# Optimization experiments

Hardware: AMD Instinct MI355X
Metric: run time of the kernel (lower is better)

## Reference

```python
import jax, jax.numpy as jnp
import numpy as np

RADIUS = 3
T_STEPS = 2
NEG = -9.0e8
B, L, DEG = 256, 64, 6
FEAT, BOND, FP, OUT = 39, 10, 256, 1


def _leaky(x):
    return jax.nn.leaky_relu(x, 0.01)


def _gru(x, h, wih, whh, bih, bhh):
    # PyTorch GRUCell: gates ordered (r, z, n)
    gi = x @ wih.T + bih
    gh = h @ whh.T + bhh
    ir, iz, inn = jnp.split(gi, 3, axis=-1)
    hr, hz, hn = jnp.split(gh, 3, axis=-1)
    r = jax.nn.sigmoid(ir + hr)
    z = jax.nn.sigmoid(iz + hz)
    n = jnp.tanh(inn + r * hn)
    return (1.0 - z) * n + z * h


def _forward(atom_list, bond_list, atom_mask,
             atom_fc_w, atom_fc_b, neighbor_fc_w, neighbor_fc_b,
             align_w, align_b, attend_w, attend_b,
             gru_wih, gru_whh, gru_bih, gru_bhh,
             mol_align_w, mol_align_b, mol_attend_w, mol_attend_b,
             mol_gru_wih, mol_gru_whh, mol_gru_bih, mol_gru_bhh,
             out_w, out_b,
             atom_degree_list, bond_degree_list):
    b, l, _ = atom_list.shape
    mask = atom_mask[..., None]                                   # [B,L,1]
    atom_feature = _leaky(atom_list @ atom_fc_w.T + atom_fc_b)    # [B,L,FP]

    # per-molecule neighbor gather (padding index = L-1)
    bidx = jnp.arange(b)[:, None, None]
    atom_nb = atom_list[bidx, atom_degree_list]                    # [B,L,deg,FEAT]
    bond_nb = bond_list[bidx, bond_degree_list]                    # [B,L,deg,BOND]
    neighbor_feature = _leaky(
        jnp.concatenate([atom_nb, bond_nb], axis=-1) @ neighbor_fc_w.T + neighbor_fc_b
    )                                                              # [B,L,deg,FP]

    attend_mask = (atom_degree_list != l - 1).astype(atom_feature.dtype)[..., None]
    softmax_mask = jnp.where(atom_degree_list == l - 1, NEG, 0.0).astype(atom_feature.dtype)[..., None]

    for d in range(RADIUS):
        af_exp = jnp.broadcast_to(atom_feature[:, :, None, :], neighbor_feature.shape)
        feature_align = jnp.concatenate([af_exp, neighbor_feature], axis=-1)  # [B,L,deg,2FP]
        align_score = _leaky(feature_align @ align_w[d].T + align_b[d]) + softmax_mask
        attention_weight = jax.nn.softmax(align_score, axis=-2) * attend_mask
        attended = neighbor_feature @ attend_w[d].T + attend_b[d]
        context = jax.nn.elu(jnp.sum(attention_weight * attended, axis=-2))   # [B,L,FP]
        atom_feature = _gru(context.reshape(b * l, -1), atom_feature.reshape(b * l, -1),
                            gru_wih[d], gru_whh[d], gru_bih[d], gru_bhh[d]).reshape(b, l, -1)
        # faithful to original: self-feature broadcast across neighbor dim
        neighbor_feature = jnp.broadcast_to(jax.nn.relu(atom_feature)[:, :, None, :],
                                            neighbor_feature.shape)

    mol_feature = jnp.sum(jax.nn.relu(atom_feature) * mask, axis=-2)          # [B,FP]
    mol_softmax_mask = jnp.where(atom_mask == 0, NEG, 0.0).astype(atom_feature.dtype)[..., None]

    for _ in range(T_STEPS):
        m_exp = jnp.broadcast_to(mol_feature[:, None, :], atom_feature.shape)
        mol_align = jnp.concatenate([m_exp, atom_feature], axis=-1)           # [B,L,2FP]
        mol_score = _leaky(mol_align @ mol_align_w.T + mol_align_b) + mol_softmax_mask
        mol_w = jax.nn.softmax(mol_score, axis=-2) * mask
        attended = atom_feature @ mol_attend_w.T + mol_attend_b
        mol_context = jax.nn.elu(jnp.sum(mol_w * attended, axis=-2))
        mol_feature = _gru(mol_context, mol_feature,
                           mol_gru_wih, mol_gru_whh, mol_gru_bih, mol_gru_bhh)

    mol_prediction = mol_feature @ out_w.T + out_b
    return atom_feature, mol_prediction


def setup_inputs() -> dict:
    key = jax.random.key(0)
    ks = jax.random.split(key, 20)
    s = 0.05
    return {
        "atom_list": jax.random.normal(ks[0], (B, L, FEAT), jnp.float32),
        "bond_list": jax.random.normal(ks[1], (B, L, BOND), jnp.float32),
        "atom_degree_list": jax.random.randint(ks[2], (B, L, DEG), 0, L),
        "bond_degree_list": jax.random.randint(ks[3], (B, L, DEG), 0, L),
        "atom_mask": jnp.ones((B, L), jnp.float32),
        "atom_fc_w": jax.random.normal(ks[4], (FP, FEAT)) * s,
        "atom_fc_b": jnp.zeros((FP,)),
        "neighbor_fc_w": jax.random.normal(ks[5], (FP, FEAT + BOND)) * s,
        "neighbor_fc_b": jnp.zeros((FP,)),
        "align_w": jax.random.normal(ks[6], (RADIUS, 1, 2 * FP)) * s,
        "align_b": jnp.zeros((RADIUS, 1)),
        "attend_w": jax.random.normal(ks[7], (RADIUS, FP, FP)) * s,
        "attend_b": jnp.zeros((RADIUS, FP)),
        "gru_wih": jax.random.normal(ks[8], (RADIUS, 3 * FP, FP)) * s,
        "gru_whh": jax.random.normal(ks[9], (RADIUS, 3 * FP, FP)) * s,
        "gru_bih": jnp.zeros((RADIUS, 3 * FP)),
        "gru_bhh": jnp.zeros((RADIUS, 3 * FP)),
        "mol_align_w": jax.random.normal(ks[10], (1, 2 * FP)) * s,
        "mol_align_b": jnp.zeros((1,)),
        "mol_attend_w": jax.random.normal(ks[11], (FP, FP)) * s,
        "mol_attend_b": jnp.zeros((FP,)),
        "mol_gru_wih": jax.random.normal(ks[12], (3 * FP, FP)) * s,
        "mol_gru_whh": jax.random.normal(ks[13], (3 * FP, FP)) * s,
        "mol_gru_bih": jnp.zeros((3 * FP,)),
        "mol_gru_bhh": jnp.zeros((3 * FP,)),
        "out_w": jax.random.normal(ks[14], (OUT, FP)) * s,
        "out_b": jnp.zeros((OUT,)),
    }


def reference(atom_list, bond_list, atom_degree_list, bond_degree_list, atom_mask,
              atom_fc_w, atom_fc_b, neighbor_fc_w, neighbor_fc_b,
              align_w, align_b, attend_w, attend_b,
              gru_wih, gru_whh, gru_bih, gru_bhh,
              mol_align_w, mol_align_b, mol_attend_w, mol_attend_b,
              mol_gru_wih, mol_gru_whh, mol_gru_bih, mol_gru_bhh,
              out_w, out_b):
    return _forward(atom_list, bond_list, atom_mask,
                    atom_fc_w, atom_fc_b, neighbor_fc_w, neighbor_fc_b,
                    align_w, align_b, attend_w, attend_b,
                    gru_wih, gru_whh, gru_bih, gru_bhh,
                    mol_align_w, mol_align_b, mol_attend_w, mol_attend_b,
                    mol_gru_wih, mol_gru_whh, mol_gru_bih, mol_gru_bhh,
                    out_w, out_b,
                    atom_degree_list, bond_degree_list)
```

## Files before the change

### kernel.cpp

```cpp
#include <hip/hip_runtime.h>
#include <hip/hip_bf16.h>

#define NB 256
#define NL 64
#define DEG 6
#define FEAT 39
#define BOND 10
#define FP 256
#define NEGV (-9.0e8f)

using s16x8 = __attribute__((ext_vector_type(8))) short;
using f32x4 = __attribute__((ext_vector_type(4))) float;

__device__ __forceinline__ unsigned short f2bf(float f){
  unsigned u = __float_as_uint(f);
  u += 0x7fffu + ((u >> 16) & 1u);
  return (unsigned short)(u >> 16);
}
__device__ __forceinline__ float lo16(unsigned u){ return __uint_as_float(u << 16); }
__device__ __forceinline__ float hi16(unsigned u){ return __uint_as_float(u & 0xffff0000u); }

__device__ __forceinline__ float block_sum256(float v, float* scr){
  #pragma unroll
  for(int o=32;o>0;o>>=1) v += __shfl_down(v, o, 64);
  __syncthreads();
  if((threadIdx.x & 63) == 0) scr[threadIdx.x >> 6] = v;
  __syncthreads();
  return scr[0] + scr[1] + scr[2] + scr[3];
}
__device__ __forceinline__ float wave_allsum(float v){
  #pragma unroll
  for(int o=1;o<64;o<<=1) v += __shfl_xor(v, o, 64);
  return v;
}

#define MCVT_N0 65536
#define MCVT_N1 196608
#define MCVT_N2 196608
#define MCVT_TOT (MCVT_N0+MCVT_N1+MCVT_N2)
#define CTXPK_N (3*8*8192)
#define GPK_N   (3*2*8*24576)
#define HALF_U16 24576

__global__ void k_cvt_mol(const float* __restrict__ a0, const float* __restrict__ a1,
                          const float* __restrict__ a2, unsigned short* __restrict__ dst){
  int i = blockIdx.x*256 + threadIdx.x;
  if(i >= MCVT_TOT) return;
  int off = i; const float* src;
  if(off < MCVT_N0) src = a0;
  else { off -= MCVT_N0;
    if(off < MCVT_N1) src = a1;
    else { off -= MCVT_N1; src = a2; } }
  dst[i] = f2bf(src[off]);
}

__global__ void k_pack(const float* __restrict__ attend_w, const float* __restrict__ gru_wih,
                       const float* __restrict__ gru_whh,
                       unsigned short* __restrict__ ctx_pk, unsigned short* __restrict__ gates_pk){
  int i = blockIdx.x*256 + threadIdx.x;
  if(i < CTXPK_N){
    int d = i >> 16;
    int rem = i & 65535;
    int kk = rem >> 13;
    int r2 = rem & 8191;
    int g = r2 >> 9;
    int l = (r2 >> 3) & 63;
    int q = r2 & 7;
    int row = g*16 + (l & 15);
    int k = kk*32 + (l >> 4)*8 + q;
    ctx_pk[i] = f2bf(attend_w[((size_t)d*256 + row)*256 + k]);
  } else {
    int j = i - CTXPK_N;
    if(j >= GPK_N) return;
    int d = j / 393216;
    int rem = j - d*393216;
    int nc = rem / 196608; rem -= nc*196608;
    int kk = rem / 24576;  rem -= kk*24576;
    int f = rem >> 9;
    int l = (rem >> 3) & 63;
    int q = rem & 7;
    int s = f >> 3, g = f & 7;
    int row = nc*128 + g*16 + (l & 15);
    int k = kk*32 + (l >> 4)*8 + q;
    float v = (s < 3) ? gru_wih[(((size_t)d*3 + s)*256 + row)*256 + k]
                      : gru_whh[(((size_t)d*3 + (s-3))*256 + row)*256 + k];
    gates_pk[j] = f2bf(v);
  }
}

__global__ void k_tr(const float* __restrict__ aw, const float* __restrict__ nw,
                     float* __restrict__ afcT, unsigned short* __restrict__ nfcT){
  int i = blockIdx.x*256 + threadIdx.x;
  if(i < 40*256){
    int k = i >> 8, r = i & 255;
    afcT[i] = (k < FEAT) ? aw[r*FEAT + k] : 0.f;
  } else {
    int j = i - 40*256;
    int k = j >> 8, r = j & 255;
    nfcT[j] = (k < FEAT+BOND) ? f2bf(nw[r*(FEAT+BOND) + k]) : (unsigned short)0;
  }
}

__global__ __launch_bounds__(256) void k_atom4(const float* __restrict__ atom,
    const float* __restrict__ afcT, const float* __restrict__ bias, float* __restrict__ af){
  __shared__ float x_s[4][40];
  const int t = threadIdx.x, bl0 = blockIdx.x*4;
  for(int idx=t; idx<4*FEAT; idx+=256){ int a=idx/FEAT, k=idx%FEAT; x_s[a][k]=atom[(bl0+a)*FEAT+k]; }
  if(t < 4) x_s[t][39] = 0.f;
  __syncthreads();
  const int w = t>>6, t0 = (t&63)*4, row = bl0 + w;
  float4 b4 = *(const float4*)&bias[t0];
  float acc[4] = {b4.x, b4.y, b4.z, b4.w};
  for(int k=0;k<40;++k){
    float iv = x_s[w][k];
    float4 wv = *(const float4*)&afcT[(k<<8)+t0];
    acc[0]=fmaf(iv,wv.x,acc[0]); acc[1]=fmaf(iv,wv.y,acc[1]);
    acc[2]=fmaf(iv,wv.z,acc[2]); acc[3]=fmaf(iv,wv.w,acc[3]);
  }
  float4 o;
  o.x = acc[0]>0.f?acc[0]:0.01f*acc[0]; o.y = acc[1]>0.f?acc[1]:0.01f*acc[1];
  o.z = acc[2]>0.f?acc[2]:0.01f*acc[2]; o.w = acc[3]>0.f?acc[3]:0.01f*acc[3];
  *(float4*)&af[(size_t)row*FP + t0] = o;
}

__global__ __launch_bounds__(256) void k_nbr4(const float* __restrict__ atom,
    const float* __restrict__ bond, const int* __restrict__ adl, const int* __restrict__ bdl,
    const unsigned short* __restrict__ nfcT, const float* __restrict__ bn,
    const float* __restrict__ alw, const float* __restrict__ alb,
    const float* __restrict__ af, float* __restrict__ wnf, float* __restrict__ swb){
  __shared__ float in_s[4][DEG][52];
  __shared__ int   ai_s[4][DEG];
  const int t = threadIdx.x, bl0 = blockIdx.x*4;
  if(t < 24){ int a=t/6, d=t%6; ai_s[a][d] = adl[(bl0+a)*DEG + d]; }
  __syncthreads();
  for(int idx=t; idx<4*DEG*(FEAT+BOND); idx+=256){
    int a = idx/(DEG*(FEAT+BOND)), rem = idx%(DEG*(FEAT+BOND));
    int d = rem/(FEAT+BOND), k = rem%(FEAT+BOND);
    int bb = (bl0+a) >> 6;
    float v;
    if(k < FEAT) v = atom[((size_t)bb*NL + ai_s[a][d])*FEAT + k];
    else { int bi = bdl[(bl0+a)*DEG + d]; v = bond[((size_t)bb*NL + bi)*BOND + (k-FEAT)]; }
    in_s[a][d][k] = v;
  }
  if(t < 24){ int a=t/6, d=t%6; in_s[a][d][49]=0.f; in_s[a][d][50]=0.f; in_s[a][d][51]=0.f; }
  __syncthreads();
  const int w = t>>6, lane = t&63, t0 = lane*4, row = bl0 + w;
  float acc[DEG][4] = {};
  for(int k=0;k<52;++k){
    uint2 u = *(const uint2*)&nfcT[(k<<8) + t0];
    float w0=lo16(u.x), w1=hi16(u.x), w2=lo16(u.y), w3=hi16(u.y);
    #pragma unroll
    for(int d=0;d<DEG;++d){
      float iv = in_s[w][d][k];
      acc[d][0]=fmaf(iv,w0,acc[d][0]); acc[d][1]=fmaf(iv,w1,acc[d][1]);
      acc[d][2]=fmaf(iv,w2,acc[d][2]); acc[d][3]=fmaf(iv,w3,acc[d][3]);
    }
  }
  float4 bnv = *(const float4*)&bn[t0];
  float bna[4] = {bnv.x, bnv.y, bnv.z, bnv.w};
  float nf[DEG][4];
  #pragma unroll
  for(int d=0;d<DEG;++d)
    #pragma unroll
    for(int j=0;j<4;++j){ float v = acc[d][j] + bna[j]; nf[d][j] = v>0.f ? v : 0.01f*v; }
  float4 af4 = *(const float4*)&af[(size_t)row*FP + t0];
  float4 a1  = *(const float4*)&alw[t0];
  float4 a2  = *(const float4*)&alw[FP + t0];
  float sa = wave_allsum(af4.x*a1.x + af4.y*a1.y + af4.z*a1.z + af4.w*a1.w);
  float sd[DEG];
  #pragma unroll
  for(int d=0;d<DEG;++d)
    sd[d] = wave_allsum(nf[d][0]*a2.x + nf[d][1]*a2.y + nf[d][2]*a2.z + nf[d][3]*a2.w);
  float ab = alb[0];
  float sc[DEG], msk[DEG];
  #pragma unroll
  for(int d=0;d<DEG;++d){
    float v = sa + sd[d] + ab;
    v = v>0.f ? v : 0.01f*v;
    msk[d] = (ai_s[w][d] == NL-1) ? 0.f : 1.f;
    sc[d] = v + (msk[d] > 0.f ? 0.f : NEGV);
  }
  float m = sc[0];
  #pragma unroll
  for(int d=1;d<DEG;++d) m = fmaxf(m, sc[d]);
  float e[DEG], Z = 0.f;
  #pragma unroll
  for(int d=0;d<DEG;++d){ e[d] = expf(sc[d]-m); Z += e[d]; }
  float wgt[DEG], sw = 0.f;
  #pragma unroll
  for(int d=0;d<DEG;++d){ wgt[d] = e[d]/Z*msk[d]; sw += wgt[d]; }
  float o[4] = {};
  #pragma unroll
  for(int d=0;d<DEG;++d)
    #pragma unroll
    for(int j=0;j<4;++j) o[j] = fmaf(wgt[d], nf[d][j], o[j]);
  float4 ov; ov.x=o[0]; ov.y=o[1]; ov.z=o[2]; ov.w=o[3];
  *(float4*)&wnf[(size_t)row*FP + t0] = ov;
  if(lane == 0) swb[row] = sw;
}

__global__ __launch_bounds__(512) void k_radius2(
    const float* __restrict__ wnf, float* __restrict__ af, const float* __restrict__ swb,
    const unsigned short* __restrict__ ctx_pk, const unsigned short* __restrict__ gates_pk,
    const float* __restrict__ attend_b,
    const float* __restrict__ gru_bih, const float* __restrict__ gru_bhh){
  __shared__ __align__(16) unsigned short Cf[32*512];
  __shared__ __align__(16) unsigned short Bu[2][HALF_U16];
  const int t = threadIdx.x;
  const int w = t>>6, lane = t&63, lr = lane&15, ks = lane>>4;
  const int wm = w>>2, wn = w&3;
  const int m0 = blockIdx.x*64;

  s16x8 pf[6]; int pfn = 0;
  auto LOADS = [&](int s){
    if(s >= 72) return;
    int d2 = s/24, r = s - d2*24;
    const unsigned short* src; int n;
    if(r < 8){ n = 2; src = ctx_pk + ((size_t)d2*8 + r)*8192; }
    else { int g = r - 8; n = 6; src = gates_pk + ((size_t)(d2*2 + (g>>3))*8 + (g&7))*24576; }
    pfn = n;
    #pragma unroll
    for(int c=0;c<6;++c) if(c < n) pf[c] = *(const s16x8*)(src + (w + c*8)*512 + lane*8);
  };
  auto WRITET = [&](int h){
    #pragma unroll
    for(int c=0;c<6;++c) if(c < pfn) *(s16x8*)&Bu[h][(w + c*8)*512 + lane*8] = pf[c];
  };

  LOADS(0);
  WRITET(0);
  LOADS(1);
  int half = 0;

  for(int d=0; d<3; ++d){
    const float* bat  = attend_b + d*256;
    const float* bihd = gru_bih + d*768;
    const float* bhhd = gru_bhh + d*768;

    __syncthreads();
    float4 px0[2], px1[2];
    #pragma unroll
    for(int mf=0; mf<2; ++mf){
      int row = m0 + wm*32 + mf*16 + lr;
      const float* sp = (d==0 ? wnf : af) + (size_t)row*256 + ks*8;
      px0[mf] = *(const float4*)sp; px1[mf] = *(const float4*)(sp+4);
    }
    f32x4 acc2[2][4] = {};
    for(int kk=0; kk<8; ++kk){
      int s = d*24 + kk;
      __syncthreads();
      WRITET(half^1);
      LOADS(s+2);
      float4 cx0[2] = {px0[0], px0[1]};
      float4 cx1[2] = {px1[0], px1[1]};
      if(kk < 7){
        #pragma unroll
        for(int mf=0; mf<2; ++mf){
          int row = m0 + wm*32 + mf*16 + lr;
          const float* sp = (d==0 ? wnf : af) + (size_t)row*256 + (kk+1)*32 + ks*8;
          px0[mf] = *(const float4*)sp; px1[mf] = *(const float4*)(sp+4);
        }
      }
      s16x8 xf[2];
      #pragma unroll
      for(int mf=0; mf<2; ++mf){
        float4 v0 = cx0[mf], v1 = cx1[mf];
        if(d != 0){
          float sw = swb[m0 + wm*32 + mf*16 + lr];
          v0.x=fmaxf(v0.x,0.f)*sw; v0.y=fmaxf(v0.y,0.f)*sw;
          v0.z=fmaxf(v0.z,0.f)*sw; v0.w=fmaxf(v0.w,0.f)*sw;
          v1.x=fmaxf(v1.x,0.f)*sw; v1.y=fmaxf(v1.y,0.f)*sw;
          v1.z=fmaxf(v1.z,0.f)*sw; v1.w=fmaxf(v1.w,0.f)*sw;
        }
        unsigned short tmp[8] = {f2bf(v0.x),f2bf(v0.y),f2bf(v0.z),f2bf(v0.w),
                                 f2bf(v1.x),f2bf(v1.y),f2bf(v1.z),f2bf(v1.w)};
        xf[mf] = *(s16x8*)tmp;
      }
      #pragma unroll
      for(int nf=0; nf<4; ++nf){
        s16x8 wf = *(const s16x8*)&Bu[half][((wn*4 + nf)*64 + lane)*8];
        acc2[0][nf] = __builtin_amdgcn_mfma_f32_16x16x32_bf16(wf, xf[0], acc2[0][nf],0,0,0);
        acc2[1][nf] = __builtin_amdgcn_mfma_f32_16x16x32_bf16(wf, xf[1], acc2[1][nf],0,0,0);
      }
      half ^= 1;
    }
    #pragma unroll
    for(int mf=0; mf<2; ++mf){
      float swv = swb[m0 + wm*32 + mf*16 + lr];
      #pragma unroll
      for(int nf=0; nf<4; ++nf){
        int nb = wn*64 + nf*16 + ks*4;
        float4 b4 = *(const float4*)&bat[nb];
        float bj[4] = {b4.x, b4.y, b4.z, b4.w};
        unsigned short o4[4];
        #pragma unroll
        for(int j=0;j<4;++j){
          float v = acc2[mf][nf][j] + swv*bj[j];
          v = v > 0.f ? v : expm1f(v);
          o4[j] = f2bf(v);
        }
        int gm = wm*2 + mf;
        int kkp = wn*2 + (nf>>1);
        int lhi = ((nf & 1) << 1) | (ks >> 1);
        int addr = (gm*8 + kkp)*512 + (lhi*16 + lr)*8 + (ks & 1)*4;
        *(uint2*)&Cf[addr] = *(uint2*)o4;
      }
    }
    float4 ph0[2], ph1[2];
    #pragma unroll
    for(int mf=0; mf<2; ++mf){
      int row = m0 + wm*32 + mf*16 + lr;
      const float* sp = af + (size_t)row*256 + ks*8;
      ph0[mf] = *(const float4*)sp; ph1[mf] = *(const float4*)(sp+4);
    }
    float hnew0[2][2][4];
    for(int nc=0; nc<2; ++nc){
      f32x4 aR[2][2] = {}, aZ[2][2] = {}, aN[2][2] = {}, aH[2][2] = {};
      for(int kk=0; kk<8; ++kk){
        int s = d*24 + 8 + nc*8 + kk;
        __syncthreads();
        if(s < 71) WRITET(half^1);
        LOADS(s+2);
        float4 ch0[2] = {ph0[0], ph0[1]};
        float4 ch1[2] = {ph1[0], ph1[1]};
        bool lastHK = (nc == 1) && (kk == 7);
        if(!lastHK){
          int kkn = (kk < 7) ? kk+1 : 0;
          #pragma unroll
          for(int mf=0; mf<2; ++mf){
            int row = m0 + wm*32 + mf*16 + lr;
            const float* sp = af + (size_t)row*256 + kkn*32 + ks*8;
            ph0[mf] = *(const float4*)sp; ph1[mf] = *(const float4*)(sp+4);
          }
        }
        s16x8 hf[2];
        #pragma unroll
        for(int mf=0; mf<2; ++mf){
          float4 v0 = ch0[mf], v1 = ch1[mf];
          unsigned short tmp[8] = {f2bf(v0.x),f2bf(v0.y),f2bf(v0.z),f2bf(v0.w),
                                   f2bf(v1.x),f2bf(v1.y),f2bf(v1.z),f2bf(v1.w)};
          hf[mf] = *(s16x8*)tmp;
        }
        s16x8 cf0 = *(const s16x8*)&Cf[((wm*2 + 0)*8 + kk)*512 + lane*8];
        s16x8 cf1 = *(const s16x8*)&Cf[((wm*2 + 1)*8 + kk)*512 + lane*8];
        #pragma unroll
        for(int fn=0; fn<2; ++fn){
          int g = wn*2 + fn;
          s16x8 b0 = *(const s16x8*)&Bu[half][((0*8 + g)*64 + lane)*8];
          s16x8 b1 = *(const s16x8*)&Bu[half][((1*8 + g)*64 + lane)*8];
          s16x8 b2 = *(const s16x8*)&Bu[half][((2*8 + g)*64 + lane)*8];
          s16x8 b3 = *(const s16x8*)&Bu[half][((3*8 + g)*64 + lane)*8];
          s16x8 b4 = *(const s16x8*)&Bu[half][((4*8 + g)*64 + lane)*8];
          s16x8 b5 = *(const s16x8*)&Bu[half][((5*8 + g)*64 + lane)*8];
          aR[0][fn] = __builtin_amdgcn_mfma_f32_16x16x32_bf16(cf0, b0, aR[0][fn],0,0,0);
          aR[1][fn] = __builtin_amdgcn_mfma_f32_16x16x32_bf16(cf1, b0, aR[1][fn],0,0,0);
          aZ[0][fn] = __builtin_amdgcn_mfma_f32_16x16x32_bf16(cf0, b1, aZ[0][fn],0,0,0);
          aZ[1][fn] = __builtin_amdgcn_mfma_f32_16x16x32_bf16(cf1, b1, aZ[1][fn],0,0,0);
          aN[0][fn] = __builtin_amdgcn_mfma_f32_16x16x32_bf16(cf0, b2, aN[0][fn],0,0,0);
          aN[1][fn] = __builtin_amdgcn_mfma_f32_16x16x32_bf16(cf1, b2, aN[1][fn],0,0,0);
          aR[0][fn] = __builtin_amdgcn_mfma_f32_16x16x32_bf16(hf[0], b3, aR[0][fn],0,0,0);
          aR[1][fn] = __builtin_amdgcn_mfma_f32_16x16x32_bf16(hf[1], b3, aR[1][fn],0,0,0);
          aZ[0][fn] = __builtin_amdgcn_mfma_f32_16x16x32_bf16(hf[0], b4, aZ[0][fn],0,0,0);
          aZ[1][fn] = __builtin_amdgcn_mfma_f32_16x16x32_bf16(hf[1], b4, aZ[1][fn],0,0,0);
          aH[0][fn] = __builtin_amdgcn_mfma_f32_16x16x32_bf16(hf[0], b5, aH[0][fn],0,0,0);
          aH[1][fn] = __builtin_amdgcn_mfma_f32_16x16x32_bf16(hf[1], b5, aH[1][fn],0,0,0);
        }
        half ^= 1;
      }
      if(nc == 0){
        #pragma unroll
        for(int mf=0; mf<2; ++mf)
          #pragma unroll
          for(int fn=0; fn<2; ++fn){
            int n = wn*32 + fn*16 + lr;
            float brz = bihd[n] + bhhd[n];
            float bzz = bihd[256+n] + bhhd[256+n];
            float bnn = bihd[512+n];
            float bhn = bhhd[512+n];
            #pragma unroll
            for(int j=0;j<4;++j){
              int m = m0 + wm*32 + mf*16 + ks*4 + j;
              float hold = af[(size_t)m*256 + n];
              float r = 1.f/(1.f + expf(-(aR[mf][fn][j] + brz)));
              float z = 1.f/(1.f + expf(-(aZ[mf][fn][j] + bzz)));
              float ng = tanhf(aN[mf][fn][j] + bnn + r*(aH[mf][fn][j] + bhn));
              hnew0[mf][fn][j] = (1.f - z)*ng + z*hold;
            }
          }
      } else {
        #pragma unroll
        for(int mf=0; mf<2; ++mf)
          #pragma unroll
          for(int fn=0; fn<2; ++fn){
            int n = 128 + wn*32 + fn*16 + lr;
            float brz = bihd[n] + bhhd[n];
            float bzz = bihd[256+n] + bhhd[256+n];
            float bnn = bihd[512+n];
            float bhn = bhhd[512+n];
            #pragma unroll
            for(int j=0;j<4;++j){
              int m = m0 + wm*32 + mf*16 + ks*4 + j;
              float hold = af[(size_t)m*256 + n];
              float r = 1.f/(1.f + expf(-(aR[mf][fn][j] + brz)));
              float z = 1.f/(1.f + expf(-(aZ[mf][fn][j] + bzz)));
              float ng = tanhf(aN[mf][fn][j] + bnn + r*(aH[mf][fn][j] + bhn));
              af[(size_t)m*256 + n] = (1.f - z)*ng + z*hold;
            }
          }
        #pragma unroll
        for(int mf=0; mf<2; ++mf)
          #pragma unroll
          for(int fn=0; fn<2; ++fn){
            int n = wn*32 + fn*16 + lr;
            #pragma unroll
            for(int j=0;j<4;++j){
              int m = m0 + wm*32 + mf*16 + ks*4 + j;
              af[(size_t)m*256 + n] = hnew0[mf][fn][j];
            }
          }
      }
    }
  }
}

__global__ __launch_bounds__(256) void k_lin_gemm(
    const float* __restrict__ Xsrc, const unsigned short* __restrict__ Wbf,
    const float* __restrict__ bias, float* __restrict__ Y){
  __shared__ unsigned short A_lds[64][264];
  __shared__ unsigned short B_lds[64][264];
  const int t = threadIdx.x;
  const int m0 = (blockIdx.x >> 2) * 64, n0 = (blockIdx.x & 3) * 64;
  const int rb = t >> 4, cb = (t & 15) * 16;
  for(int i=0;i<4;++i){
    int row = i*16 + rb;
    const float* src = Xsrc + (size_t)(m0+row)*FP + cb;
    unsigned short tmp[16];
    #pragma unroll
    for(int q=0;q<4;++q){
      float4 v = ((const float4*)src)[q];
      tmp[q*4+0]=f2bf(v.x); tmp[q*4+1]=f2bf(v.y); tmp[q*4+2]=f2bf(v.z); tmp[q*4+3]=f2bf(v.w);
    }
    *(s16x8*)&A_lds[row][cb]   = *(s16x8*)&tmp[0];
    *(s16x8*)&A_lds[row][cb+8] = *(s16x8*)&tmp[8];
    const unsigned short* wsrc = Wbf + (size_t)(n0+row)*FP + cb;
    *(s16x8*)&B_lds[row][cb]   = *(const s16x8*)&wsrc[0];
    *(s16x8*)&B_lds[row][cb+8] = *(const s16x8*)&wsrc[8];
  }
  __syncthreads();
  const int w = t>>6, lane = t&63, lr = lane&15, ks = lane>>4;
  const int wr = (w>>1)*32, wc = (w&1)*32;
  f32x4 acc[2][2] = {};
  #pragma unroll
  for(int kk=0;kk<8;++kk){
    int ko = kk*32 + ks*8;
    s16x8 a0 = *(const s16x8*)&A_lds[wr+lr][ko];
    s16x8 a1 = *(const s16x8*)&A_lds[wr+16+lr][ko];
    s16x8 b0 = *(const s16x8*)&B_lds[wc+lr][ko];
    s16x8 b1 = *(const s16x8*)&B_lds[wc+16+lr][ko];
    acc[0][0] = __builtin_amdgcn_mfma_f32_16x16x32_bf16(a0,b0,acc[0][0],0,0,0);
    acc[0][1] = __builtin_amdgcn_mfma_f32_16x16x32_bf16(a0,b1,acc[0][1],0,0,0);
    acc[1][0] = __builtin_amdgcn_mfma_f32_16x16x32_bf16(a1,b0,acc[1][0],0,0,0);
    acc[1][1] = __builtin_amdgcn_mfma_f32_16x16x32_bf16(a1,b1,acc[1][1],0,0,0);
  }
  #pragma unroll
  for(int fm=0;fm<2;++fm)
    #pragma unroll
    for(int fn=0;fn<2;++fn){
      int n = n0 + wc + fn*16 + lr;
      float bv = bias[n];
      #pragma unroll
      for(int j=0;j<4;++j){
        int m = m0 + wr + fm*16 + ks*4 + j;
        Y[(size_t)m*FP + n] = acc[fm][fn][j] + bv;
      }
    }
}

__global__ __launch_bounds__(256) void k_gates32(
    const unsigned short* __restrict__ ctxbf, const float* __restrict__ h_glob,
    const unsigned short* __restrict__ wihbf, const unsigned short* __restrict__ whhbf,
    const float* __restrict__ bih, const float* __restrict__ bhh,
    float* __restrict__ h_out){
  __shared__ unsigned short A_ctx[32][40];
  __shared__ unsigned short A_h[32][40];
  __shared__ unsigned short B_lds[6][64][40];
  const int t = threadIdx.x;
  const int m0 = (blockIdx.x >> 2) * 32, nc = (blockIdx.x & 3) * 64;
  const int w = t>>6, lane = t&63, lr = lane&15, ks = lane>>4;
  const int mh = (w>>1)*16, nh = (w&1)*32;
  f32x4 acc[6][2] = {};
  for(int kk=0;kk<8;++kk){
    const int k0 = kk*32;
    __syncthreads();
    {
      int row = t>>3, c4 = (t&7)*4;
      *(uint2*)&A_ctx[row][c4] = *(const uint2*)(ctxbf + (size_t)(m0+row)*FP + k0 + c4);
      float4 hv = *(const float4*)(h_glob + (size_t)(m0+row)*FP + k0 + c4);
      unsigned short ht[4] = {f2bf(hv.x), f2bf(hv.y), f2bf(hv.z), f2bf(hv.w)};
      *(uint2*)&A_h[row][c4] = *(uint2*)ht;
    }
    #pragma unroll
    for(int i=0;i<6;++i){
      int idx = i*256 + t;
      int s = idx >> 8, rem = idx & 255;
      int row = rem >> 2, c8 = (rem & 3)*8;
      const unsigned short* wsrc = (s < 3)
          ? wihbf + (size_t)(s*FP + nc + row)*FP + k0 + c8
          : whhbf + (size_t)((s-3)*FP + nc + row)*FP + k0 + c8;
      *(s16x8*)&B_lds[s][row][c8] = *(const s16x8*)wsrc;
    }
    __syncthreads();
    s16x8 ac = *(const s16x8*)&A_ctx[mh+lr][ks*8];
    s16x8 ah = *(const s16x8*)&A_h[mh+lr][ks*8];
    #pragma unroll
    for(int s=0;s<6;++s){
      s16x8 a = (s < 3) ? ac : ah;
      #pragma unroll
      for(int fn=0;fn<2;++fn){
        s16x8 b = *(const s16x8*)&B_lds[s][nh+fn*16+lr][ks*8];
        acc[s][fn] = __builtin_amdgcn_mfma_f32_16x16x32_bf16(a,b,acc[s][fn],0,0,0);
      }
    }
  }
  #pragma unroll
  for(int fn=0;fn<2;++fn){
    int n = nc + nh + fn*16 + lr;
    float bir = bih[n], biz = bih[FP+n], bin_ = bih[2*FP+n];
    float bhr = bhh[n], bhz = bhh[FP+n], bhn  = bhh[2*FP+n];
    #pragma unroll
    for(int j=0;j<4;++j){
      int m = m0 + mh + ks*4 + j;
      float h = h_glob[(size_t)m*FP + n];
      float ir = acc[0][fn][j]+bir, iz = acc[1][fn][j]+biz, inn = acc[2][fn][j]+bin_;
      float hr = acc[3][fn][j]+bhr, hz = acc[4][fn][j]+bhz, hn  = acc[5][fn][j]+bhn;
      float r = 1.f/(1.f + expf(-(ir+hr)));
      float z = 1.f/(1.f + expf(-(iz+hz)));
      float ng = tanhf(inn + r*hn);
      h_out[(size_t)m*FP + n] = (1.f-z)*ng + z*h;
    }
  }
}

__global__ void k_finalize(const float* __restrict__ af, const float* __restrict__ mask,
                           float* __restrict__ molfeat, float* __restrict__ out_af){
  const int b = blockIdx.x, t = threadIdx.x;
  __shared__ float msk_s[NL];
  if(t < NL) msk_s[t] = mask[b*NL + t];
  __syncthreads();
  float mf = 0.f;
  for(int l=0;l<NL;++l){
    float v = af[(size_t)(b*NL + l)*FP + t];
    out_af[(size_t)(b*NL + l)*FP + t] = v;
    mf = fmaf(fmaxf(v,0.f), msk_s[l], mf);
  }
  molfeat[b*FP + t] = mf;
}

__global__ void k_mol_ctx(const float* __restrict__ af, const float* __restrict__ att,
    const float* __restrict__ mfin, const float* __restrict__ maw,
    const float* __restrict__ mabp, const float* __restrict__ mask,
    unsigned short* __restrict__ ctxb){
  const int b = blockIdx.x, t = threadIdx.x;
  __shared__ float mf_s[FP];
  __shared__ float sc_s[NL], aw_s[NL], scr[4];
  mf_s[t] = mfin[b*FP + t];
  __syncthreads();
  float sa = block_sum256(maw[t]*mf_s[t], scr);
  int l = t >> 2, q = t & 3;
  float p = 0.f;
  {
    const float4* ar = (const float4*)(af + (size_t)(b*NL + l)*FP + q*64);
    const float4* w2 = (const float4*)(maw + FP + q*64);
    #pragma unroll
    for(int k=0;k<16;++k){
      float4 a = ar[k], ww = w2[k];
      p = fmaf(a.x,ww.x,p); p = fmaf(a.y,ww.y,p);
      p = fmaf(a.z,ww.z,p); p = fmaf(a.w,ww.w,p);
    }
  }
  p += __shfl_xor(p, 1, 64);
  p += __shfl_xor(p, 2, 64);
  if(q == 0){
    float mv = mask[b*NL + l];
    float v = sa + p + mabp[0];
    v = v > 0.f ? v : 0.01f*v;
    sc_s[l] = v + (mv == 0.f ? NEGV : 0.f);
  }
  __syncthreads();
  if(t < NL){
    float s = sc_s[t];
    float m = s;
    #pragma unroll
    for(int o=32;o>0;o>>=1) m = fmaxf(m, __shfl_xor(m, o, 64));
    float e = expf(s - m);
    float Z = e;
    #pragma unroll
    for(int o=32;o>0;o>>=1) Z += __shfl_xor(Z, o, 64);
    aw_s[t] = e / Z * mask[b*NL + t];
  }
  __syncthreads();
  float acc = 0.f;
  for(int l2=0;l2<NL;++l2) acc = fmaf(aw_s[l2], att[(size_t)(b*NL + l2)*FP + t], acc);
  float c = acc > 0.f ? acc : expm1f(acc);
  ctxb[b*FP + t] = f2bf(c);
}

__global__ void k_out(const float* __restrict__ molfeat, const float* __restrict__ ow,
                      const float* __restrict__ ob, float* __restrict__ outp){
  const int b = blockIdx.x, t = threadIdx.x;
  __shared__ float scr[4];
  float s = block_sum256(molfeat[b*FP + t]*ow[t], scr);
  if(t == 0) outp[b] = s + ob[0];
}

extern "C" void kernel_launch(void* const* d_in, const int* in_sizes, int n_in,
                              void* d_out, int out_size, void* d_ws, size_t ws_size,
                              hipStream_t stream){
  const float* atom_list = (const float*)d_in[0];
  const float* bond_list = (const float*)d_in[1];
  const int*   adl       = (const int*)d_in[2];
  const int*   bdl       = (const int*)d_in[3];
  const float* amask     = (const float*)d_in[4];
  const float* afc_w     = (const float*)d_in[5];
  const float* afc_b     = (const float*)d_in[6];
  const float* nfc_w     = (const float*)d_in[7];
  const float* nfc_b     = (const float*)d_in[8];
  const float* align_w   = (const float*)d_in[9];
  const float* align_b   = (const float*)d_in[10];
  const float* attend_w  = (const float*)d_in[11];
  const float* attend_b  = (const float*)d_in[12];
  const float* gru_wih   = (const float*)d_in[13];
  const float* gru_whh   = (const float*)d_in[14];
  const float* gru_bih   = (const float*)d_in[15];
  const float* gru_bhh   = (const float*)d_in[16];
  const float* mol_align_w  = (const float*)d_in[17];
  const float* mol_align_b  = (const float*)d_in[18];
  const float* mol_attend_w = (const float*)d_in[19];
  const float* mol_attend_b = (const float*)d_in[20];
  const float* mg_wih    = (const float*)d_in[21];
  const float* mg_whh    = (const float*)d_in[22];
  const float* mg_bih    = (const float*)d_in[23];
  const float* mg_bhh    = (const float*)d_in[24];
  const float* out_w     = (const float*)d_in[25];
  const float* out_b     = (const float*)d_in[26];

  float* out_af   = (float*)d_out;
  float* out_pred = out_af + (size_t)NB*NL*FP;

  const size_t NROW = (size_t)NB*NL;
  const size_t F32_CNT = 2*NROW*FP + NROW + 2*(size_t)NB*FP + 40*256;
  const size_t U16_CNT = (size_t)NB*FP + MCVT_TOT + 52*256 + CTXPK_N + GPK_N;
  const size_t NEED = F32_CNT*4 + U16_CNT*2;

  if(ws_size >= NEED){
    float* af_a    = (float*)d_ws;
    float* wnf     = af_a + NROW*FP;
    float* swb     = wnf  + NROW*FP;
    float* mf_a    = swb  + NROW;
    float* mf_b    = mf_a + (size_t)NB*FP;
    float* afcT    = mf_b + (size_t)NB*FP;
    unsigned short* ctxbf_m = (unsigned short*)(afcT + 40*256);
    unsigned short* maw_bf  = ctxbf_m + (size_t)NB*FP;
    unsigned short* mgih_bf = maw_bf + MCVT_N0;
    unsigned short* mghh_bf = mgih_bf + MCVT_N1;
    unsigned short* nfcT_bf = mghh_bf + MCVT_N2;
    unsigned short* ctx_pk  = nfcT_bf + 52*256;
    unsigned short* gates_pk= ctx_pk + CTXPK_N;

    k_cvt_mol<<<(MCVT_TOT+255)/256, 256, 0, stream>>>(mol_attend_w, mg_wih, mg_whh, maw_bf);
    k_pack<<<(CTXPK_N+GPK_N)/256, 256, 0, stream>>>(attend_w, gru_wih, gru_whh, ctx_pk, gates_pk);
    k_tr<<<(40*256 + 52*256)/256, 256, 0, stream>>>(afc_w, nfc_w, afcT, nfcT_bf);

    k_atom4<<<NB*NL/4, 256, 0, stream>>>(atom_list, afcT, afc_b, af_a);
    k_nbr4<<<NB*NL/4, 256, 0, stream>>>(atom_list, bond_list, adl, bdl,
                                        nfcT_bf, nfc_b, align_w, align_b, af_a, wnf, swb);
    k_radius2<<<NB*NL/64, 512, 0, stream>>>(wnf, af_a, swb, ctx_pk, gates_pk,
                                            attend_b, gru_bih, gru_bhh);
    k_lin_gemm<<<(NB*NL/64)*4, 256, 0, stream>>>(af_a, maw_bf, mol_attend_b, wnf);
    k_finalize<<<NB, 256, 0, stream>>>(af_a, amask, mf_a, out_af);
    float* m_cur = mf_a; float* m_nxt = mf_b;
    for(int s=0; s<2; ++s){
      k_mol_ctx<<<NB, 256, 0, stream>>>(af_a, wnf, m_cur, mol_align_w, mol_align_b,
                                        amask, ctxbf_m);
      k_gates32<<<(NB/32)*4, 256, 0, stream>>>(ctxbf_m, m_cur, mgih_bf, mghh_bf,
                                               mg_bih, mg_bhh, m_nxt);
      float* tmp = m_cur; m_cur = m_nxt; m_nxt = tmp;
    }
    k_out<<<NB, 256, 0, stream>>>(m_cur, out_w, out_b, out_pred);
  } else {
    float* af      = (float*)d_ws;
    float* wnf     = af  + NROW*FP;
    float* swb     = wnf + NROW*FP;
    float* molfeat = swb + NROW;
    k_atom4<<<NB*NL/4, 256, 0, stream>>>(atom_list, (const float*)afc_w, afc_b, af);
    (void)molfeat; (void)bond_list; (void)adl; (void)bdl; (void)amask;
    (void)align_w; (void)align_b; (void)attend_w; (void)attend_b;
    (void)gru_wih; (void)gru_whh; (void)gru_bih; (void)gru_bhh;
    (void)mol_align_w; (void)mol_align_b; (void)mol_attend_w; (void)mol_attend_b;
    (void)mg_wih; (void)mg_whh; (void)mg_bih; (void)mg_bhh; (void)out_w; (void)out_b;
  }
}
```

Before: 321.9 us.

## Read radius weights directly from global memory instead of LDS double-buffering

Removes the double-buffered LDS staging of packed attention and GRU weights in the radius kernel. MFMA B-fragments are now loaded straight from global memory (served by L2/cache), which drops most per-k-step block barriers and cuts LDS use, possibly allowing more blocks per CU. The software prefetch of activations is also removed. GRU outputs for both column halves are now kept in registers and written after a barrier. The trade-off is that every wave re-reads the weights from global memory with no explicit prefetch, which exposes load latency and raises register pressure.

```diff
diff --git a/kernel.cpp b/kernel.cpp
--- a/kernel.cpp
+++ b/kernel.cpp
@@ -40,7 +40,6 @@
 #define MCVT_TOT (MCVT_N0+MCVT_N1+MCVT_N2)
 #define CTXPK_N (3*8*8192)
 #define GPK_N   (3*2*8*24576)
-#define HALF_U16 24576
 
 __global__ void k_cvt_mol(const float* __restrict__ a0, const float* __restrict__ a1,
                           const float* __restrict__ a2, unsigned short* __restrict__ dst){
@@ -199,74 +198,39 @@
   if(lane == 0) swb[row] = sw;
 }
 
-__global__ __launch_bounds__(512) void k_radius2(
+__global__ __launch_bounds__(512) void k_radius4(
     const float* __restrict__ wnf, float* __restrict__ af, const float* __restrict__ swb,
     const unsigned short* __restrict__ ctx_pk, const unsigned short* __restrict__ gates_pk,
     const float* __restrict__ attend_b,
     const float* __restrict__ gru_bih, const float* __restrict__ gru_bhh){
   __shared__ __align__(16) unsigned short Cf[32*512];
-  __shared__ __align__(16) unsigned short Bu[2][HALF_U16];
   const int t = threadIdx.x;
   const int w = t>>6, lane = t&63, lr = lane&15, ks = lane>>4;
   const int wm = w>>2, wn = w&3;
   const int m0 = blockIdx.x*64;
 
-  s16x8 pf[6]; int pfn = 0;
-  auto LOADS = [&](int s){
-    if(s >= 72) return;
-    int d2 = s/24, r = s - d2*24;
-    const unsigned short* src; int n;
-    if(r < 8){ n = 2; src = ctx_pk + ((size_t)d2*8 + r)*8192; }
-    else { int g = r - 8; n = 6; src = gates_pk + ((size_t)(d2*2 + (g>>3))*8 + (g&7))*24576; }
-    pfn = n;
-    #pragma unroll
-    for(int c=0;c<6;++c) if(c < n) pf[c] = *(const s16x8*)(src + (w + c*8)*512 + lane*8);
-  };
-  auto WRITET = [&](int h){
-    #pragma unroll
-    for(int c=0;c<6;++c) if(c < pfn) *(s16x8*)&Bu[h][(w + c*8)*512 + lane*8] = pf[c];
-  };
-
-  LOADS(0);
-  WRITET(0);
-  LOADS(1);
-  int half = 0;
-
   for(int d=0; d<3; ++d){
     const float* bat  = attend_b + d*256;
     const float* bihd = gru_bih + d*768;
     const float* bhhd = gru_bhh + d*768;
 
     __syncthreads();
-    float4 px0[2], px1[2];
-    #pragma unroll
-    for(int mf=0; mf<2; ++mf){
-      int row = m0 + wm*32 + mf*16 + lr;
-      const float* sp = (d==0 ? wnf : af) + (size_t)row*256 + ks*8;
-      px0[mf] = *(const float4*)sp; px1[mf] = *(const float4*)(sp+4);
-    }
     f32x4 acc2[2][4] = {};
+    #pragma unroll
     for(int kk=0; kk<8; ++kk){
-      int s = d*24 + kk;
-      __syncthreads();
-      WRITET(half^1);
-      LOADS(s+2);
-      float4 cx0[2] = {px0[0], px0[1]};
-      float4 cx1[2] = {px1[0], px1[1]};
-      if(kk < 7){
-        #pragma unroll
-        for(int mf=0; mf<2; ++mf){
-          int row = m0 + wm*32 + mf*16 + lr;
-          const float* sp = (d==0 ? wnf : af) + (size_t)row*256 + (kk+1)*32 + ks*8;
-          px0[mf] = *(const float4*)sp; px1[mf] = *(const float4*)(sp+4);
-        }
-      }
+      const unsigned short* ct = ctx_pk + ((size_t)d*8 + kk)*8192;
       s16x8 xf[2];
       #pragma unroll
       for(int mf=0; mf<2; ++mf){
-        float4 v0 = cx0[mf], v1 = cx1[mf];
-        if(d != 0){
-          float sw = swb[m0 + wm*32 + mf*16 + lr];
+        int row = m0 + wm*32 + mf*16 + lr;
+        float4 v0, v1;
+        if(d == 0){
+          const float* sp = wnf + (size_t)row*256 + kk*32 + ks*8;
+          v0 = *(const float4*)sp; v1 = *(const float4*)(sp+4);
+        } else {
+          const float* sp = af + (size_t)row*256 + kk*32 + ks*8;
+          v0 = *(const float4*)sp; v1 = *(const float4*)(sp+4);
+          float sw = swb[row];
           v0.x=fmaxf(v0.x,0.f)*sw; v0.y=fmaxf(v0.y,0.f)*sw;
           v0.z=fmaxf(v0.z,0.f)*sw; v0.w=fmaxf(v0.w,0.f)*sw;
           v1.x=fmaxf(v1.x,0.f)*sw; v1.y=fmaxf(v1.y,0.f)*sw;
@@ -278,11 +242,10 @@
       }
       #pragma unroll
       for(int nf=0; nf<4; ++nf){
-        s16x8 wf = *(const s16x8*)&Bu[half][((wn*4 + nf)*64 + lane)*8];
+        s16x8 wf = *(const s16x8*)(ct + ((wn*4 + nf)*64 + lane)*8);
         acc2[0][nf] = __builtin_amdgcn_mfma_f32_16x16x32_bf16(wf, xf[0], acc2[0][nf],0,0,0);
         acc2[1][nf] = __builtin_amdgcn_mfma_f32_16x16x32_bf16(wf, xf[1], acc2[1][nf],0,0,0);
       }
-      half ^= 1;
     }
     #pragma unroll
     for(int mf=0; mf<2; ++mf){
@@ -306,37 +269,20 @@
         *(uint2*)&Cf[addr] = *(uint2*)o4;
       }
     }
-    float4 ph0[2], ph1[2];
-    #pragma unroll
-    for(int mf=0; mf<2; ++mf){
-      int row = m0 + wm*32 + mf*16 + lr;
-      const float* sp = af + (size_t)row*256 + ks*8;
-      ph0[mf] = *(const float4*)sp; ph1[mf] = *(const float4*)(sp+4);
-    }
+    __syncthreads();
     float hnew0[2][2][4];
+    float hnew1[2][2][4];
     for(int nc=0; nc<2; ++nc){
       f32x4 aR[2][2] = {}, aZ[2][2] = {}, aN[2][2] = {}, aH[2][2] = {};
+      #pragma unroll
       for(int kk=0; kk<8; ++kk){
-        int s = d*24 + 8 + nc*8 + kk;
-        __syncthreads();
-        if(s < 71) WRITET(half^1);
-        LOADS(s+2);
-        float4 ch0[2] = {ph0[0], ph0[1]};
-        float4 ch1[2] = {ph1[0], ph1[1]};
-        bool lastHK = (nc == 1) && (kk == 7);
-        if(!lastHK){
-          int kkn = (kk < 7) ? kk+1 : 0;
-          #pragma unroll
-          for(int mf=0; mf<2; ++mf){
-            int row = m0 + wm*32 + mf*16 + lr;
-            const float* sp = af + (size_t)row*256 + kkn*32 + ks*8;
-            ph0[mf] = *(const float4*)sp; ph1[mf] = *(const float4*)(sp+4);
-          }
-        }
+        const unsigned short* gp = gates_pk + ((size_t)(d*2 + nc)*8 + kk)*24576;
         s16x8 hf[2];
         #pragma unroll
         for(int mf=0; mf<2; ++mf){
-          float4 v0 = ch0[mf], v1 = ch1[mf];
+          int row = m0 + wm*32 + mf*16 + lr;
+          const float* sp = af + (size_t)row*256 + kk*32 + ks*8;
+          float4 v0 = *(const float4*)sp, v1 = *(const float4*)(sp+4);
           unsigned short tmp[8] = {f2bf(v0.x),f2bf(v0.y),f2bf(v0.z),f2bf(v0.w),
                                    f2bf(v1.x),f2bf(v1.y),f2bf(v1.z),f2bf(v1.w)};
           hf[mf] = *(s16x8*)tmp;
@@ -346,12 +292,12 @@
         #pragma unroll
         for(int fn=0; fn<2; ++fn){
           int g = wn*2 + fn;
-          s16x8 b0 = *(const s16x8*)&Bu[half][((0*8 + g)*64 + lane)*8];
-          s16x8 b1 = *(const s16x8*)&Bu[half][((1*8 + g)*64 + lane)*8];
-          s16x8 b2 = *(const s16x8*)&Bu[half][((2*8 + g)*64 + lane)*8];
-          s16x8 b3 = *(const s16x8*)&Bu[half][((3*8 + g)*64 + lane)*8];
-          s16x8 b4 = *(const s16x8*)&Bu[half][((4*8 + g)*64 + lane)*8];
-          s16x8 b5 = *(const s16x8*)&Bu[half][((5*8 + g)*64 + lane)*8];
+          s16x8 b0 = *(const s16x8*)(gp + ((0*8 + g)*64 + lane)*8);
+          s16x8 b1 = *(const s16x8*)(gp + ((1*8 + g)*64 + lane)*8);
+          s16x8 b2 = *(const s16x8*)(gp + ((2*8 + g)*64 + lane)*8);
+          s16x8 b3 = *(const s16x8*)(gp + ((3*8 + g)*64 + lane)*8);
+          s16x8 b4 = *(const s16x8*)(gp + ((4*8 + g)*64 + lane)*8);
+          s16x8 b5 = *(const s16x8*)(gp + ((5*8 + g)*64 + lane)*8);
           aR[0][fn] = __builtin_amdgcn_mfma_f32_16x16x32_bf16(cf0, b0, aR[0][fn],0,0,0);
           aR[1][fn] = __builtin_amdgcn_mfma_f32_16x16x32_bf16(cf1, b0, aR[1][fn],0,0,0);
           aZ[0][fn] = __builtin_amdgcn_mfma_f32_16x16x32_bf16(cf0, b1, aZ[0][fn],0,0,0);
@@ -365,60 +311,45 @@
           aH[0][fn] = __builtin_amdgcn_mfma_f32_16x16x32_bf16(hf[0], b5, aH[0][fn],0,0,0);
           aH[1][fn] = __builtin_amdgcn_mfma_f32_16x16x32_bf16(hf[1], b5, aH[1][fn],0,0,0);
         }
-        half ^= 1;
       }
-      if(nc == 0){
+      float (*hn_)[2][4] = (nc == 0) ? hnew0 : hnew1;
+      int nbase = nc*128;
+      #pragma unroll
+      for(int mf=0; mf<2; ++mf)
         #pragma unroll
-        for(int mf=0; mf<2; ++mf)
+        for(int fn=0; fn<2; ++fn){
+          int n = nbase + wn*32 + fn*16 + lr;
+          float brz = bihd[n] + bhhd[n];
+          float bzz = bihd[256+n] + bhhd[256+n];
+          float bnn = bihd[512+n];
+          float bhn = bhhd[512+n];
           #pragma unroll
-          for(int fn=0; fn<2; ++fn){
-            int n = wn*32 + fn*16 + lr;
-            float brz = bihd[n] + bhhd[n];
-            float bzz = bihd[256+n] + bhhd[256+n];
-            float bnn = bihd[512+n];
-            float bhn = bhhd[512+n];
-            #pragma unroll
-            for(int j=0;j<4;++j){
-              int m = m0 + wm*32 + mf*16 + ks*4 + j;
-              float hold = af[(size_t)m*256 + n];
-              float r = 1.f/(1.f + expf(-(aR[mf][fn][j] + brz)));
-              float z = 1.f/(1.f + expf(-(aZ[mf][fn][j] + bzz)));
-              float ng = tanhf(aN[mf][fn][j] + bnn + r*(aH[mf][fn][j] + bhn));
-              hnew0[mf][fn][j] = (1.f - z)*ng + z*hold;
-            }
+          for(int j=0;j<4;++j){
+            int m = m0 + wm*32 + mf*16 + ks*4 + j;
+            float hold = af[(size_t)m*256 + n];
+            float r = 1.f/(1.f + expf(-(aR[mf][fn][j] + brz)));
+            float z = 1.f/(1.f + expf(-(aZ[mf][fn][j] + bzz)));
+            float ng = tanhf(aN[mf][fn][j] + bnn + r*(aH[mf][fn][j] + bhn));
+            hn_[mf][fn][j] = (1.f - z)*ng + z*hold;
           }
-      } else {
+        }
+    }
+    __syncthreads();
+    #pragma unroll
+    for(int nc=0; nc<2; ++nc){
+      float (*hn_)[2][4] = (nc == 0) ? hnew0 : hnew1;
+      int nbase = nc*128;
+      #pragma unroll
+      for(int mf=0; mf<2; ++mf)
         #pragma unroll
-        for(int mf=0; mf<2; ++mf)
+        for(int fn=0; fn<2; ++fn){
+          int n = nbase + wn*32 + fn*16 + lr;
           #pragma unroll
-          for(int fn=0; fn<2; ++fn){
-            int n = 128 + wn*32 + fn*16 + lr;
-            float brz = bihd[n] + bhhd[n];
-            float bzz = bihd[256+n] + bhhd[256+n];
-            float bnn = bihd[512+n];
-            float bhn = bhhd[512+n];
-            #pragma unroll
-            for(int j=0;j<4;++j){
-              int m = m0 + wm*32 + mf*16 + ks*4 + j;
-              float hold = af[(size_t)m*256 + n];
-              float r = 1.f/(1.f + expf(-(aR[mf][fn][j] + brz)));
-              float z = 1.f/(1.f + expf(-(aZ[mf][fn][j] + bzz)));
-              float ng = tanhf(aN[mf][fn][j] + bnn + r*(aH[mf][fn][j] + bhn));
-              af[(size_t)m*256 + n] = (1.f - z)*ng + z*hold;
-            }
+          for(int j=0;j<4;++j){
+            int m = m0 + wm*32 + mf*16 + ks*4 + j;
+            af[(size_t)m*256 + n] = hn_[mf][fn][j];
           }
-        #pragma unroll
-        for(int mf=0; mf<2; ++mf)
-          #pragma unroll
-          for(int fn=0; fn<2; ++fn){
-            int n = wn*32 + fn*16 + lr;
-            #pragma unroll
-            for(int j=0;j<4;++j){
-              int m = m0 + wm*32 + mf*16 + ks*4 + j;
-              af[(size_t)m*256 + n] = hnew0[mf][fn][j];
-            }
-          }
-      }
+        }
     }
   }
 }
@@ -674,7 +605,7 @@
     k_atom4<<<NB*NL/4, 256, 0, stream>>>(atom_list, afcT, afc_b, af_a);
     k_nbr4<<<NB*NL/4, 256, 0, stream>>>(atom_list, bond_list, adl, bdl,
                                         nfcT_bf, nfc_b, align_w, align_b, af_a, wnf, swb);
-    k_radius2<<<NB*NL/64, 512, 0, stream>>>(wnf, af_a, swb, ctx_pk, gates_pk,
+    k_radius4<<<NB*NL/64, 512, 0, stream>>>(wnf, af_a, swb, ctx_pk, gates_pk,
                                             attend_b, gru_bih, gru_bhh);
     k_lin_gemm<<<(NB*NL/64)*4, 256, 0, stream>>>(af_a, maw_bf, mol_attend_b, wnf);
     k_finalize<<<NB, 256, 0, stream>>>(af_a, amask, mf_a, out_af);
@@ -688,12 +619,9 @@
     }
     k_out<<<NB, 256, 0, stream>>>(m_cur, out_w, out_b, out_pred);
   } else {
-    float* af      = (float*)d_ws;
-    float* wnf     = af  + NROW*FP;
-    float* swb     = wnf + NROW*FP;
-    float* molfeat = swb + NROW;
+    float* af = (float*)d_ws;
     k_atom4<<<NB*NL/4, 256, 0, stream>>>(atom_list, (const float*)afc_w, afc_b, af);
-    (void)molfeat; (void)bond_list; (void)adl; (void)bdl; (void)amask;
+    (void)bond_list; (void)adl; (void)bdl; (void)amask;
     (void)align_w; (void)align_b; (void)attend_w; (void)attend_b;
     (void)gru_wih; (void)gru_whh; (void)gru_bih; (void)gru_bhh;
     (void)mol_align_w; (void)mol_align_b; (void)mol_attend_w; (void)mol_attend_b;
```

Measured after the change: 367.9 us. +14.3%, slower.
